# Kernel optimization log

Hardware: AMD Instinct MI355X
Metric: run time of the kernel (lower is better)

The kernel has to match this reference:

```python
import jax, jax.numpy as jnp
import numpy as np

D_MODEL = 1024
NUM_HEADS = 16
HEAD_DIM = D_MODEL // NUM_HEADS

def setup_inputs() -> dict:
    key = jax.random.key(0)
    ks = jax.random.split(key, 9)
    B, L = 2, 2048
    s = 1.0 / np.sqrt(D_MODEL)
    return {
        "x":  jax.random.normal(ks[0], (B, L, D_MODEL), dtype=jnp.float32),
        "Wq": jax.random.uniform(ks[1], (D_MODEL, D_MODEL), jnp.float32, -s, s),
        "bq": jax.random.uniform(ks[2], (D_MODEL,), jnp.float32, -s, s),
        "Wk": jax.random.uniform(ks[3], (D_MODEL, D_MODEL), jnp.float32, -s, s),
        "bk": jax.random.uniform(ks[4], (D_MODEL,), jnp.float32, -s, s),
        "Wv": jax.random.uniform(ks[5], (D_MODEL, D_MODEL), jnp.float32, -s, s),
        "bv": jax.random.uniform(ks[6], (D_MODEL,), jnp.float32, -s, s),
        "Wo": jax.random.uniform(ks[7], (D_MODEL, D_MODEL), jnp.float32, -s, s),
        "bo": jax.random.uniform(ks[8], (D_MODEL,), jnp.float32, -s, s),
    }

def _split_heads(t):
    B, L, _ = t.shape
    return t.reshape(B, L, NUM_HEADS, HEAD_DIM).transpose(0, 2, 1, 3)  # [B,H,L,Dh]

def reference(x, Wq, bq, Wk, bk, Wv, bv, Wo, bo):
    # Linear projections (torch Linear: y = x @ W.T + b)
    Q = _split_heads(x @ Wq.T + bq)
    K = _split_heads(x @ Wk.T + bk)
    V = _split_heads(x @ Wv.T + bv)
    scale = 1.0 / jnp.sqrt(jnp.asarray(HEAD_DIM, dtype=x.dtype))
    scores = jnp.einsum('bhqd,bhkd->bhqk', Q, K) * scale  # [B,H,L,L]
    attn_weights = jax.nn.softmax(scores, axis=-1)
    ctx = jnp.einsum('bhqk,bhkd->bhqd', attn_weights, V)  # [B,H,L,Dh]
    B, H, L, Dh = ctx.shape
    ctx = ctx.transpose(0, 2, 1, 3).reshape(B, L, H * Dh)
    out = ctx @ Wo.T + bo  # dropout p=0.0 -> identity
    return (out, attn_weights)
```

## Files before the change

### kernel.cpp

```cpp
#include <hip/hip_runtime.h>

typedef unsigned short u16;
typedef __bf16 bf16x8 __attribute__((ext_vector_type(8)));
typedef float f32x4 __attribute__((ext_vector_type(4)));

#define WSTR 72
#define TSZ (64 * WSTR)

__device__ __forceinline__ u16 f2bf(float f) {
    union { float f; unsigned int u; } v; v.f = f;
    unsigned int u = v.u;
    u += 0x7fffu + ((u >> 16) & 1u);
    return (u16)(u >> 16);
}

__device__ __forceinline__ u16 cvt_bf(float f) {
    __bf16 h = (__bf16)f;
    union { __bf16 h; u16 u; } v; v.h = h; return v.u;
}

__device__ __forceinline__ void gload16(const u16* g, u16* l) {
    __builtin_amdgcn_global_load_lds((const __attribute__((address_space(1))) unsigned int*)(const void*)g,
                                     (__attribute__((address_space(3))) unsigned int*)(void*)l, 16, 0, 0);
}

#define MFMA16(A, B, C) __builtin_amdgcn_mfma_f32_16x16x32_bf16(A, B, C, 0, 0, 0)

#define LGKM_BARRIER() do { \
    asm volatile("s_waitcnt lgkmcnt(0)\n\ts_barrier" ::: "memory"); \
    __builtin_amdgcn_sched_barrier(0); \
} while (0)

__global__ __launch_bounds__(256) void k_cvtX(const float* __restrict__ src, u16* __restrict__ dst) {
    const size_t i = ((size_t)blockIdx.x * 256 + threadIdx.x) * 8;
    float4 v0 = *(const float4*)(src + i);
    float4 v1 = *(const float4*)(src + i + 4);
    u16 o[8];
    o[0] = f2bf(v0.x); o[1] = f2bf(v0.y); o[2] = f2bf(v0.z); o[3] = f2bf(v0.w);
    o[4] = f2bf(v1.x); o[5] = f2bf(v1.y); o[6] = f2bf(v1.z); o[7] = f2bf(v1.w);
    *(uint4*)(dst + i) = *(const uint4*)o;
}

__global__ __launch_bounds__(256) void k_cvtW(const float* __restrict__ w0, const float* __restrict__ w1,
                                              const float* __restrict__ w2, const float* __restrict__ w3,
                                              u16* __restrict__ dst) {
    const int z = blockIdx.z;
    const float* src = z == 0 ? w0 : z == 1 ? w1 : z == 2 ? w2 : w3;
    const size_t i = ((size_t)blockIdx.x * 256 + threadIdx.x) * 8;
    float4 v0 = *(const float4*)(src + i);
    float4 v1 = *(const float4*)(src + i + 4);
    u16 o[8];
    o[0] = f2bf(v0.x); o[1] = f2bf(v0.y); o[2] = f2bf(v0.z); o[3] = f2bf(v0.w);
    o[4] = f2bf(v1.x); o[5] = f2bf(v1.y); o[6] = f2bf(v1.z); o[7] = f2bf(v1.w);
    *(uint4*)(dst + (size_t)z * 1048576 + i) = *(const uint4*)o;
}

__global__ __launch_bounds__(256) void k_qkv(const u16* __restrict__ Xb, const u16* __restrict__ Wb,
                                             const float* __restrict__ bq, const float* __restrict__ bk,
                                             const float* __restrict__ bv,
                                             u16* __restrict__ Q, u16* __restrict__ Kd, u16* __restrict__ Vtmp) {
    __shared__ __align__(16) u16 lA[128 * 32];
    __shared__ __align__(16) u16 lB[128 * 32];
    const int t = threadIdx.x;
    const int n0 = blockIdx.x * 128;
    const int m0 = blockIdx.y * 128;
    const int lane = t & 63, wave = t >> 6;
    const int wm = (wave >> 1) * 64, wn = (wave & 1) * 64;
    const int quad = lane >> 4, m16 = lane & 15;
    const int r4 = t >> 2, c8 = (t & 3) * 8;
    f32x4 acc[4][4] = {};
    for (int k0 = 0; k0 < 1024; k0 += 32) {
        gload16(Xb + (size_t)(m0 + r4) * 1024 + k0 + c8,       &lA[t * 8]);
        gload16(Xb + (size_t)(m0 + 64 + r4) * 1024 + k0 + c8,  &lA[2048 + t * 8]);
        gload16(Wb + (size_t)(n0 + r4) * 1024 + k0 + c8,       &lB[t * 8]);
        gload16(Wb + (size_t)(n0 + 64 + r4) * 1024 + k0 + c8,  &lB[2048 + t * 8]);
        __syncthreads();
        bf16x8 af[4], bfr[4];
#pragma unroll
        for (int i = 0; i < 4; ++i) {
            af[i]  = *(const bf16x8*)(lA + (wm + i * 16 + m16) * 32 + quad * 8);
            bfr[i] = *(const bf16x8*)(lB + (wn + i * 16 + m16) * 32 + quad * 8);
        }
#pragma unroll
        for (int mi = 0; mi < 4; ++mi)
#pragma unroll
            for (int ni = 0; ni < 4; ++ni)
                acc[mi][ni] = MFMA16(af[mi], bfr[ni], acc[mi][ni]);
        __syncthreads();
    }
#pragma unroll
    for (int ni = 0; ni < 4; ++ni) {
        const int gcol = n0 + wn + ni * 16 + m16;
        const int mat = gcol >> 10;
        const int col = gcol & 1023;
        const int h = col >> 6, d = col & 63;
        const float bias = (mat == 0 ? bq : mat == 1 ? bk : bv)[col];
        u16* dst = mat == 0 ? Q : mat == 1 ? Kd : Vtmp;
#pragma unroll
        for (int mi = 0; mi < 4; ++mi)
#pragma unroll
            for (int e = 0; e < 4; ++e) {
                const int row = m0 + wm + mi * 16 + quad * 4 + e;
                const int b = row >> 11, l = row & 2047;
                dst[(((size_t)(b * 16 + h)) * 2048 + l) * 64 + d] = cvt_bf(acc[mi][ni][e] + bias);
            }
    }
}

__global__ __launch_bounds__(256) void k_vtr(const u16* __restrict__ Vtmp, u16* __restrict__ Vt) {
    __shared__ __align__(16) u16 ld[64 * WSTR];
    const int t = threadIdx.x;
    const int bh = blockIdx.y;
    const int l0 = blockIdx.x * 64;
    const int r = t >> 3, c8 = (t & 7) * 8;
    const u16* src = Vtmp + (size_t)bh * 2048 * 64 + (size_t)l0 * 64;
    *(uint4*)&ld[r * WSTR + c8]        = *(const uint4*)(src + (size_t)r * 64 + c8);
    *(uint4*)&ld[(r + 32) * WSTR + c8] = *(const uint4*)(src + (size_t)(r + 32) * 64 + c8);
    __syncthreads();
    u16* dst = Vt + (size_t)bh * 64 * 2048 + l0;
#pragma unroll
    for (int half = 0; half < 2; ++half) {
        const int d = r + half * 32;
        u16 p[8];
#pragma unroll
        for (int i = 0; i < 8; ++i) p[i] = ld[(c8 + i) * WSTR + d];
        *(uint4*)(dst + (size_t)d * 2048 + c8) = *(const uint4*)p;
    }
}

__global__ __launch_bounds__(256) void k_attn(const u16* __restrict__ Q,
                                              const u16* __restrict__ K,
                                              const u16* __restrict__ Vt,
                                              float* __restrict__ attn,
                                              u16* __restrict__ ctx) {
    __shared__ __align__(16) u16 lK[2 * TSZ];
    __shared__ __align__(16) u16 lV[2 * TSZ];
    __shared__ __align__(16) u16 lW[2 * TSZ];
    __shared__ float sred[2][64];
    const int t = threadIdx.x;
    const int bh = blockIdx.x;
    const int m0 = blockIdx.y * 64;
    const int lane = t & 63, wave = t >> 6;
    const int wq = (wave & 1) * 32;
    const int wk = (wave >> 1) * 32;
    const int wm = (wave >> 1) * 32, wn = (wave & 1) * 32;
    const int quad = lane >> 4, m16 = lane & 15;
    const int sr = t >> 3, sc = (t & 7) * 8;
    const u16* Qh = Q + (size_t)bh * 2048 * 64;
    const u16* Kh = K + (size_t)bh * 2048 * 64;
    const u16* Vh = Vt + (size_t)bh * 64 * 2048;
    float* ah = attn + ((size_t)bh << 22) + (size_t)m0 * 2048;

    const float SC = 0.18033688011112042f;

    bf16x8 qf[2][2];
#pragma unroll
    for (int ni = 0; ni < 2; ++ni)
#pragma unroll
        for (int ks = 0; ks < 2; ++ks)
            qf[ni][ks] = *(const bf16x8*)(Qh + (size_t)(m0 + wq + ni * 16 + m16) * 64 + ks * 32 + quad * 8);

    float slane[2] = {0.f, 0.f};
    {
        *(uint4*)&lK[sr * WSTR + sc]        = *(const uint4*)(Kh + (size_t)sr * 64 + sc);
        *(uint4*)&lK[(sr + 32) * WSTR + sc] = *(const uint4*)(Kh + (size_t)(sr + 32) * 64 + sc);
        int buf = 0;
        for (int kt = 0; kt < 32; ++kt) {
            LGKM_BARRIER();
            uint4 kr0, kr1;
            if (kt < 31) {
                const u16* kp = Kh + (size_t)(kt + 1) * 64 * 64;
                kr0 = *(const uint4*)(kp + (size_t)sr * 64 + sc);
                kr1 = *(const uint4*)(kp + (size_t)(sr + 32) * 64 + sc);
            }
            const u16* lKb = &lK[buf * TSZ];
            bf16x8 k00 = *(const bf16x8*)(lKb + (wk + m16) * WSTR + quad * 8);
            bf16x8 k01 = *(const bf16x8*)(lKb + (wk + m16) * WSTR + 32 + quad * 8);
            bf16x8 k10 = *(const bf16x8*)(lKb + (wk + 16 + m16) * WSTR + quad * 8);
            bf16x8 k11 = *(const bf16x8*)(lKb + (wk + 16 + m16) * WSTR + 32 + quad * 8);
            f32x4 sacc[2][2] = {};
            sacc[0][0] = MFMA16(k00, qf[0][0], sacc[0][0]);
            sacc[0][1] = MFMA16(k00, qf[1][0], sacc[0][1]);
            sacc[1][0] = MFMA16(k10, qf[0][0], sacc[1][0]);
            sacc[1][1] = MFMA16(k10, qf[1][0], sacc[1][1]);
            sacc[0][0] = MFMA16(k01, qf[0][1], sacc[0][0]);
            sacc[0][1] = MFMA16(k01, qf[1][1], sacc[0][1]);
            sacc[1][0] = MFMA16(k11, qf[0][1], sacc[1][0]);
            sacc[1][1] = MFMA16(k11, qf[1][1], sacc[1][1]);
#pragma unroll
            for (int mi = 0; mi < 2; ++mi)
#pragma unroll
                for (int e = 0; e < 4; ++e) {
                    slane[0] += __builtin_amdgcn_exp2f(sacc[mi][0][e] * SC);
                    slane[1] += __builtin_amdgcn_exp2f(sacc[mi][1][e] * SC);
                }
            if (kt < 31) {
                u16* dK = &lK[(buf ^ 1) * TSZ];
                *(uint4*)&dK[sr * WSTR + sc]        = kr0;
                *(uint4*)&dK[(sr + 32) * WSTR + sc] = kr1;
            }
            buf ^= 1;
        }
    }
#pragma unroll
    for (int ni = 0; ni < 2; ++ni) {
        slane[ni] += __shfl_xor(slane[ni], 16);
        slane[ni] += __shfl_xor(slane[ni], 32);
    }
    __syncthreads();
    if (quad == 0) {
        sred[wave >> 1][wq + m16]      = slane[0];
        sred[wave >> 1][wq + 16 + m16] = slane[1];
    }
    __syncthreads();
    float inv[2];
    inv[0] = 1.0f / (sred[0][wq + m16]      + sred[1][wq + m16]);
    inv[1] = 1.0f / (sred[0][wq + 16 + m16] + sred[1][wq + 16 + m16]);

    unsigned aoff[2][2], lwoff[2][2];
#pragma unroll
    for (int mi = 0; mi < 2; ++mi)
#pragma unroll
        for (int ni = 0; ni < 2; ++ni) {
            const int q = wq + ni * 16 + m16;
            const int k = wk + mi * 16 + quad * 4;
            aoff[mi][ni]  = (unsigned)(q * 2048 + k);
            lwoff[mi][ni] = (unsigned)(q * WSTR + k);
        }

    f32x4 cacc[2][2] = {};
    bf16x8 vp00 = {}, vp01 = {}, vp10 = {}, vp11 = {};
    {
        *(uint4*)&lK[sr * WSTR + sc]        = *(const uint4*)(Kh + (size_t)sr * 64 + sc);
        *(uint4*)&lK[(sr + 32) * WSTR + sc] = *(const uint4*)(Kh + (size_t)(sr + 32) * 64 + sc);
        *(uint4*)&lV[sr * WSTR + sc]        = *(const uint4*)(Vh + (size_t)sr * 2048 + sc);
        *(uint4*)&lV[(sr + 32) * WSTR + sc] = *(const uint4*)(Vh + (size_t)(sr + 32) * 2048 + sc);
        int buf = 0;
        for (int kt = 0; kt < 32; ++kt) {
            LGKM_BARRIER();
            uint4 kr0, kr1, vr0, vr1;
            if (kt < 31) {
                const u16* kp  = Kh + (size_t)(kt + 1) * 64 * 64;
                const u16* vp2 = Vh + (size_t)(kt + 1) * 64;
                kr0 = *(const uint4*)(kp + (size_t)sr * 64 + sc);
                kr1 = *(const uint4*)(kp + (size_t)(sr + 32) * 64 + sc);
                vr0 = *(const uint4*)(vp2 + (size_t)sr * 2048 + sc);
                vr1 = *(const uint4*)(vp2 + (size_t)(sr + 32) * 2048 + sc);
            }
            const u16* lKb = &lK[buf * TSZ];
            const u16* lVb = &lV[buf * TSZ];
            bf16x8 vn00 = *(const bf16x8*)(lVb + (wn + m16) * WSTR + quad * 8);
            bf16x8 vn01 = *(const bf16x8*)(lVb + (wn + m16) * WSTR + 32 + quad * 8);
            bf16x8 vn10 = *(const bf16x8*)(lVb + (wn + 16 + m16) * WSTR + quad * 8);
            bf16x8 vn11 = *(const bf16x8*)(lVb + (wn + 16 + m16) * WSTR + 32 + quad * 8);
            bf16x8 k00 = *(const bf16x8*)(lKb + (wk + m16) * WSTR + quad * 8);
            bf16x8 k01 = *(const bf16x8*)(lKb + (wk + m16) * WSTR + 32 + quad * 8);
            bf16x8 k10 = *(const bf16x8*)(lKb + (wk + 16 + m16) * WSTR + quad * 8);
            bf16x8 k11 = *(const bf16x8*)(lKb + (wk + 16 + m16) * WSTR + 32 + quad * 8);
            f32x4 sacc[2][2] = {};
            sacc[0][0] = MFMA16(k00, qf[0][0], sacc[0][0]);
            sacc[0][1] = MFMA16(k00, qf[1][0], sacc[0][1]);
            sacc[1][0] = MFMA16(k10, qf[0][0], sacc[1][0]);
            sacc[1][1] = MFMA16(k10, qf[1][0], sacc[1][1]);
            sacc[0][0] = MFMA16(k01, qf[0][1], sacc[0][0]);
            sacc[0][1] = MFMA16(k01, qf[1][1], sacc[0][1]);
            sacc[1][0] = MFMA16(k11, qf[0][1], sacc[1][0]);
            sacc[1][1] = MFMA16(k11, qf[1][1], sacc[1][1]);
#pragma unroll
            for (int mi = 0; mi < 2; ++mi)
#pragma unroll
                for (int ni = 0; ni < 2; ++ni)
#pragma unroll
                    for (int e = 0; e < 4; ++e)
                        sacc[mi][ni][e] = __builtin_amdgcn_exp2f(sacc[mi][ni][e] * SC) * inv[ni];
            u16* lwb = &lW[(kt & 1) * TSZ];
#pragma unroll
            for (int mi = 0; mi < 2; ++mi)
#pragma unroll
                for (int ni = 0; ni < 2; ++ni) {
                    u16 p[4];
                    p[0] = cvt_bf(sacc[mi][ni][0]); p[1] = cvt_bf(sacc[mi][ni][1]);
                    p[2] = cvt_bf(sacc[mi][ni][2]); p[3] = cvt_bf(sacc[mi][ni][3]);
                    *(uint2*)&lwb[lwoff[mi][ni]] = *(const uint2*)p;
                }
            float* ap = ah + kt * 64;
#pragma unroll
            for (int mi = 0; mi < 2; ++mi)
#pragma unroll
                for (int ni = 0; ni < 2; ++ni)
                    *(f32x4*)(ap + aoff[mi][ni]) = sacc[mi][ni];
            if (kt < 31) {
                u16* dK = &lK[(buf ^ 1) * TSZ];
                u16* dV = &lV[(buf ^ 1) * TSZ];
                *(uint4*)&dK[sr * WSTR + sc]        = kr0;
                *(uint4*)&dK[(sr + 32) * WSTR + sc] = kr1;
                *(uint4*)&dV[sr * WSTR + sc]        = vr0;
                *(uint4*)&dV[(sr + 32) * WSTR + sc] = vr1;
            }
            if (kt > 0) {
                const u16* lwp = &lW[((kt - 1) & 1) * TSZ];
                bf16x8 a00 = *(const bf16x8*)(lwp + (wm + m16) * WSTR + quad * 8);
                bf16x8 a01 = *(const bf16x8*)(lwp + (wm + m16) * WSTR + 32 + quad * 8);
                bf16x8 a10 = *(const bf16x8*)(lwp + (wm + 16 + m16) * WSTR + quad * 8);
                bf16x8 a11 = *(const bf16x8*)(lwp + (wm + 16 + m16) * WSTR + 32 + quad * 8);
                cacc[0][0] = MFMA16(a00, vp00, cacc[0][0]);
                cacc[0][1] = MFMA16(a00, vp10, cacc[0][1]);
                cacc[1][0] = MFMA16(a10, vp00, cacc[1][0]);
                cacc[1][1] = MFMA16(a10, vp10, cacc[1][1]);
                cacc[0][0] = MFMA16(a01, vp01, cacc[0][0]);
                cacc[0][1] = MFMA16(a01, vp11, cacc[0][1]);
                cacc[1][0] = MFMA16(a11, vp01, cacc[1][0]);
                cacc[1][1] = MFMA16(a11, vp11, cacc[1][1]);
            }
            vp00 = vn00; vp01 = vn01; vp10 = vn10; vp11 = vn11;
            buf ^= 1;
        }
        __syncthreads();
        const u16* lwp = &lW[(31 & 1) * TSZ];
        bf16x8 a00 = *(const bf16x8*)(lwp + (wm + m16) * WSTR + quad * 8);
        bf16x8 a01 = *(const bf16x8*)(lwp + (wm + m16) * WSTR + 32 + quad * 8);
        bf16x8 a10 = *(const bf16x8*)(lwp + (wm + 16 + m16) * WSTR + quad * 8);
        bf16x8 a11 = *(const bf16x8*)(lwp + (wm + 16 + m16) * WSTR + 32 + quad * 8);
        cacc[0][0] = MFMA16(a00, vp00, cacc[0][0]);
        cacc[0][1] = MFMA16(a00, vp10, cacc[0][1]);
        cacc[1][0] = MFMA16(a10, vp00, cacc[1][0]);
        cacc[1][1] = MFMA16(a10, vp10, cacc[1][1]);
        cacc[0][0] = MFMA16(a01, vp01, cacc[0][0]);
        cacc[0][1] = MFMA16(a01, vp11, cacc[0][1]);
        cacc[1][0] = MFMA16(a11, vp01, cacc[1][0]);
        cacc[1][1] = MFMA16(a11, vp11, cacc[1][1]);
    }

    const int b = bh >> 4, h = bh & 15;
    u16* cp = ctx + ((size_t)b * 2048) * 1024 + h * 64;
#pragma unroll
    for (int mi = 0; mi < 2; ++mi)
#pragma unroll
        for (int ni = 0; ni < 2; ++ni)
#pragma unroll
            for (int e = 0; e < 4; ++e) {
                const int row = m0 + wm + mi * 16 + quad * 4 + e;
                const int col = wn + ni * 16 + m16;
                cp[(size_t)row * 1024 + col] = cvt_bf(cacc[mi][ni][e]);
            }
}

__global__ __launch_bounds__(256) void k_out(const u16* __restrict__ ctx,
                                             const u16* __restrict__ WoB,
                                             const float* __restrict__ bo,
                                             float* __restrict__ out) {
    __shared__ __align__(16) u16 lA[128 * 32];
    __shared__ __align__(16) u16 lB[128 * 32];
    const int t = threadIdx.x;
    const int n0 = blockIdx.x * 128;
    const int m0 = blockIdx.y * 128;
    const int lane = t & 63, wave = t >> 6;
    const int wm = (wave >> 1) * 64, wn = (wave & 1) * 64;
    const int quad = lane >> 4, m16 = lane & 15;
    const int r4 = t >> 2, c8 = (t & 3) * 8;
    f32x4 acc[4][4] = {};
    for (int k0 = 0; k0 < 1024; k0 += 32) {
        gload16(ctx + (size_t)(m0 + r4) * 1024 + k0 + c8,       &lA[t * 8]);
        gload16(ctx + (size_t)(m0 + 64 + r4) * 1024 + k0 + c8,  &lA[2048 + t * 8]);
        gload16(WoB + (size_t)(n0 + r4) * 1024 + k0 + c8,       &lB[t * 8]);
        gload16(WoB + (size_t)(n0 + 64 + r4) * 1024 + k0 + c8,  &lB[2048 + t * 8]);
        __syncthreads();
        bf16x8 af[4], bfr[4];
#pragma unroll
        for (int i = 0; i < 4; ++i) {
            af[i]  = *(const bf16x8*)(lA + (wm + i * 16 + m16) * 32 + quad * 8);
            bfr[i] = *(const bf16x8*)(lB + (wn + i * 16 + m16) * 32 + quad * 8);
        }
#pragma unroll
        for (int mi = 0; mi < 4; ++mi)
#pragma unroll
            for (int ni = 0; ni < 4; ++ni)
                acc[mi][ni] = MFMA16(af[mi], bfr[ni], acc[mi][ni]);
        __syncthreads();
    }
#pragma unroll
    for (int ni = 0; ni < 4; ++ni) {
        const int col = n0 + wn + ni * 16 + m16;
        const float bv = bo[col];
#pragma unroll
        for (int mi = 0; mi < 4; ++mi)
#pragma unroll
            for (int e = 0; e < 4; ++e) {
                const int row = m0 + wm + mi * 16 + quad * 4 + e;
                out[(size_t)row * 1024 + col] = acc[mi][ni][e] + bv;
            }
    }
}

extern "C" void kernel_launch(void* const* d_in, const int* in_sizes, int n_in,
                              void* d_out, int out_size, void* d_ws, size_t ws_size,
                              hipStream_t stream) {
    const float* x  = (const float*)d_in[0];
    const float* Wq = (const float*)d_in[1];
    const float* bq = (const float*)d_in[2];
    const float* Wk = (const float*)d_in[3];
    const float* bk = (const float*)d_in[4];
    const float* Wv = (const float*)d_in[5];
    const float* bv = (const float*)d_in[6];
    const float* Wo = (const float*)d_in[7];
    const float* bo = (const float*)d_in[8];

    float* out_f = (float*)d_out;
    float* attn  = out_f + (size_t)4096 * 1024;

    u16* Xb = (u16*)d_ws;
    u16* Wb = Xb + (size_t)4194304;
    u16* Qb = Wb + (size_t)4194304;
    u16* Kb = Qb + (size_t)4194304;
    u16* Vt = Kb + (size_t)4194304;
    u16* Vtmp = (u16*)attn;

    dim3 blk(256);
    k_cvtX<<<dim3(2048), blk, 0, stream>>>(x, Xb);
    k_cvtW<<<dim3(512, 1, 4), blk, 0, stream>>>(Wq, Wk, Wv, Wo, Wb);
    k_qkv<<<dim3(24, 32), blk, 0, stream>>>(Xb, Wb, bq, bk, bv, Qb, Kb, Vtmp);
    k_vtr<<<dim3(32, 32), blk, 0, stream>>>(Vtmp, Vt);
    k_attn<<<dim3(32, 32), blk, 0, stream>>>(Qb, Kb, Vt, attn, Xb);
    k_out<<<dim3(8, 32), blk, 0, stream>>>(Xb, Wb + (size_t)3072 * 1024, bo, out_f);
}
```

Measured before the change: 693.6 us.

## Load V fragments directly from global, add MFMA priority and nontemporal stores

Removes the LDS staging buffer for V in the attention kernel and instead loads each wave's V fragments straight from global memory per tile. This frees shared memory and drops the LDS stores and reads for V, and the launch bound is raised to request three blocks per CU. The change also raises wave priority around the MFMA groups and switches the attention-weight and output stores to nontemporal stores to reduce cache pollution. The cost is less coalesced, higher-latency global loads for V that now sit on the critical path each iteration, plus added register pressure from the occupancy hint.

```diff
diff --git a/kernel.cpp b/kernel.cpp
--- a/kernel.cpp
+++ b/kernel.cpp
@@ -128,13 +128,12 @@
     }
 }
 
-__global__ __launch_bounds__(256) void k_attn(const u16* __restrict__ Q,
-                                              const u16* __restrict__ K,
-                                              const u16* __restrict__ Vt,
-                                              float* __restrict__ attn,
-                                              u16* __restrict__ ctx) {
+__global__ __launch_bounds__(256, 3) void k_attn(const u16* __restrict__ Q,
+                                                 const u16* __restrict__ K,
+                                                 const u16* __restrict__ Vt,
+                                                 float* __restrict__ attn,
+                                                 u16* __restrict__ ctx) {
     __shared__ __align__(16) u16 lK[2 * TSZ];
-    __shared__ __align__(16) u16 lV[2 * TSZ];
     __shared__ __align__(16) u16 lW[2 * TSZ];
     __shared__ float sred[2][64];
     const int t = threadIdx.x;
@@ -160,6 +159,8 @@
         for (int ks = 0; ks < 2; ++ks)
             qf[ni][ks] = *(const bf16x8*)(Qh + (size_t)(m0 + wq + ni * 16 + m16) * 64 + ks * 32 + quad * 8);
 
+    const u16* vpl = Vh + (size_t)(wn + m16) * 2048 + quad * 8;
+
     float slane[2] = {0.f, 0.f};
     {
         *(uint4*)&lK[sr * WSTR + sc]        = *(const uint4*)(Kh + (size_t)sr * 64 + sc);
@@ -179,6 +180,7 @@
             bf16x8 k10 = *(const bf16x8*)(lKb + (wk + 16 + m16) * WSTR + quad * 8);
             bf16x8 k11 = *(const bf16x8*)(lKb + (wk + 16 + m16) * WSTR + 32 + quad * 8);
             f32x4 sacc[2][2] = {};
+            __builtin_amdgcn_s_setprio(1);
             sacc[0][0] = MFMA16(k00, qf[0][0], sacc[0][0]);
             sacc[0][1] = MFMA16(k00, qf[1][0], sacc[0][1]);
             sacc[1][0] = MFMA16(k10, qf[0][0], sacc[1][0]);
@@ -187,6 +189,7 @@
             sacc[0][1] = MFMA16(k01, qf[1][1], sacc[0][1]);
             sacc[1][0] = MFMA16(k11, qf[0][1], sacc[1][0]);
             sacc[1][1] = MFMA16(k11, qf[1][1], sacc[1][1]);
+            __builtin_amdgcn_s_setprio(0);
 #pragma unroll
             for (int mi = 0; mi < 2; ++mi)
 #pragma unroll
@@ -233,31 +236,27 @@
     {
         *(uint4*)&lK[sr * WSTR + sc]        = *(const uint4*)(Kh + (size_t)sr * 64 + sc);
         *(uint4*)&lK[(sr + 32) * WSTR + sc] = *(const uint4*)(Kh + (size_t)(sr + 32) * 64 + sc);
-        *(uint4*)&lV[sr * WSTR + sc]        = *(const uint4*)(Vh + (size_t)sr * 2048 + sc);
-        *(uint4*)&lV[(sr + 32) * WSTR + sc] = *(const uint4*)(Vh + (size_t)(sr + 32) * 2048 + sc);
         int buf = 0;
         for (int kt = 0; kt < 32; ++kt) {
             LGKM_BARRIER();
-            uint4 kr0, kr1, vr0, vr1;
+            uint4 kr0, kr1;
             if (kt < 31) {
-                const u16* kp  = Kh + (size_t)(kt + 1) * 64 * 64;
-                const u16* vp2 = Vh + (size_t)(kt + 1) * 64;
+                const u16* kp = Kh + (size_t)(kt + 1) * 64 * 64;
                 kr0 = *(const uint4*)(kp + (size_t)sr * 64 + sc);
                 kr1 = *(const uint4*)(kp + (size_t)(sr + 32) * 64 + sc);
-                vr0 = *(const uint4*)(vp2 + (size_t)sr * 2048 + sc);
-                vr1 = *(const uint4*)(vp2 + (size_t)(sr + 32) * 2048 + sc);
-            }
+            }
+            const u16* vb = vpl + kt * 64;
+            bf16x8 vn00 = *(const bf16x8*)(vb);
+            bf16x8 vn01 = *(const bf16x8*)(vb + 32);
+            bf16x8 vn10 = *(const bf16x8*)(vb + 16 * 2048);
+            bf16x8 vn11 = *(const bf16x8*)(vb + 16 * 2048 + 32);
             const u16* lKb = &lK[buf * TSZ];
-            const u16* lVb = &lV[buf * TSZ];
-            bf16x8 vn00 = *(const bf16x8*)(lVb + (wn + m16) * WSTR + quad * 8);
-            bf16x8 vn01 = *(const bf16x8*)(lVb + (wn + m16) * WSTR + 32 + quad * 8);
-            bf16x8 vn10 = *(const bf16x8*)(lVb + (wn + 16 + m16) * WSTR + quad * 8);
-            bf16x8 vn11 = *(const bf16x8*)(lVb + (wn + 16 + m16) * WSTR + 32 + quad * 8);
             bf16x8 k00 = *(const bf16x8*)(lKb + (wk + m16) * WSTR + quad * 8);
             bf16x8 k01 = *(const bf16x8*)(lKb + (wk + m16) * WSTR + 32 + quad * 8);
             bf16x8 k10 = *(const bf16x8*)(lKb + (wk + 16 + m16) * WSTR + quad * 8);
             bf16x8 k11 = *(const bf16x8*)(lKb + (wk + 16 + m16) * WSTR + 32 + quad * 8);
             f32x4 sacc[2][2] = {};
+            __builtin_amdgcn_s_setprio(1);
             sacc[0][0] = MFMA16(k00, qf[0][0], sacc[0][0]);
             sacc[0][1] = MFMA16(k00, qf[1][0], sacc[0][1]);
             sacc[1][0] = MFMA16(k10, qf[0][0], sacc[1][0]);
@@ -266,6 +265,7 @@
             sacc[0][1] = MFMA16(k01, qf[1][1], sacc[0][1]);
             sacc[1][0] = MFMA16(k11, qf[0][1], sacc[1][0]);
             sacc[1][1] = MFMA16(k11, qf[1][1], sacc[1][1]);
+            __builtin_amdgcn_s_setprio(0);
 #pragma unroll
             for (int mi = 0; mi < 2; ++mi)
 #pragma unroll
@@ -288,14 +288,11 @@
             for (int mi = 0; mi < 2; ++mi)
 #pragma unroll
                 for (int ni = 0; ni < 2; ++ni)
-                    *(f32x4*)(ap + aoff[mi][ni]) = sacc[mi][ni];
+                    __builtin_nontemporal_store(sacc[mi][ni], (f32x4*)(ap + aoff[mi][ni]));
             if (kt < 31) {
                 u16* dK = &lK[(buf ^ 1) * TSZ];
-                u16* dV = &lV[(buf ^ 1) * TSZ];
                 *(uint4*)&dK[sr * WSTR + sc]        = kr0;
                 *(uint4*)&dK[(sr + 32) * WSTR + sc] = kr1;
-                *(uint4*)&dV[sr * WSTR + sc]        = vr0;
-                *(uint4*)&dV[(sr + 32) * WSTR + sc] = vr1;
             }
             if (kt > 0) {
                 const u16* lwp = &lW[((kt - 1) & 1) * TSZ];
@@ -303,6 +300,7 @@
                 bf16x8 a01 = *(const bf16x8*)(lwp + (wm + m16) * WSTR + 32 + quad * 8);
                 bf16x8 a10 = *(const bf16x8*)(lwp + (wm + 16 + m16) * WSTR + quad * 8);
                 bf16x8 a11 = *(const bf16x8*)(lwp + (wm + 16 + m16) * WSTR + 32 + quad * 8);
+                __builtin_amdgcn_s_setprio(1);
                 cacc[0][0] = MFMA16(a00, vp00, cacc[0][0]);
                 cacc[0][1] = MFMA16(a00, vp10, cacc[0][1]);
                 cacc[1][0] = MFMA16(a10, vp00, cacc[1][0]);
@@ -311,6 +309,7 @@
                 cacc[0][1] = MFMA16(a01, vp11, cacc[0][1]);
                 cacc[1][0] = MFMA16(a11, vp01, cacc[1][0]);
                 cacc[1][1] = MFMA16(a11, vp11, cacc[1][1]);
+                __builtin_amdgcn_s_setprio(0);
             }
             vp00 = vn00; vp01 = vn01; vp10 = vn10; vp11 = vn11;
             buf ^= 1;
@@ -387,7 +386,7 @@
 #pragma unroll
             for (int e = 0; e < 4; ++e) {
                 const int row = m0 + wm + mi * 16 + quad * 4 + e;
-                out[(size_t)row * 1024 + col] = acc[mi][ni][e] + bv;
+                __builtin_nontemporal_store(acc[mi][ni][e] + bv, &out[(size_t)row * 1024 + col]);
             }
     }
 }
```

Measured after the change: 762.5 us. 1.1x slower.
